# Kernel optimization log

Hardware: AMD Instinct MI355X
Metric: run time of the kernel (lower is better)

Reference implementation:

```python
import jax, jax.numpy as jnp
import numpy as np

SHAPES = ((28, 28, 28), (14, 14, 14), (7, 7, 7))  # (D,H,W) per level, hardcoded by offset_normalizer
M, L, P = 6, 3, 4  # n_heads, n_levels, n_points


def grid_sample_3d(vol, grid):
    """Trilinear grid sample, zeros padding, align_corners=False.
    vol: (B, C, D, H, W); grid: (B, Q, 3) with xyz in [-1,1] (x->W, y->H, z->D).
    Returns (B, C, Q)."""
    B, C, D, H, W = vol.shape
    x = ((grid[..., 0] + 1.0) * W - 1.0) * 0.5
    y = ((grid[..., 1] + 1.0) * H - 1.0) * 0.5
    z = ((grid[..., 2] + 1.0) * D - 1.0) * 0.5
    x0f = jnp.floor(x); y0f = jnp.floor(y); z0f = jnp.floor(z)
    fx = x - x0f; fy = y - y0f; fz = z - z0f
    x0 = x0f.astype(jnp.int32); y0 = y0f.astype(jnp.int32); z0 = z0f.astype(jnp.int32)
    flat = vol.reshape(B, C, D * H * W)
    out = jnp.zeros((B, C, grid.shape[1]), vol.dtype)
    for dz, wz in ((0, 1.0 - fz), (1, fz)):
        for dy, wy in ((0, 1.0 - fy), (1, fy)):
            for dx, wx in ((0, 1.0 - fx), (1, fx)):
                zi = z0 + dz; yi = y0 + dy; xi = x0 + dx
                valid = (zi >= 0) & (zi < D) & (yi >= 0) & (yi < H) & (xi >= 0) & (xi < W)
                idx = (jnp.clip(zi, 0, D - 1) * H + jnp.clip(yi, 0, H - 1)) * W + jnp.clip(xi, 0, W - 1)
                g = jnp.take_along_axis(flat, idx[:, None, :], axis=2)  # (B,C,Q)
                w = (wz * wy * wx) * valid.astype(vol.dtype)
                out = out + g * w[:, None, :]
    return out


def setup_inputs() -> dict:
    key = jax.random.key(0)
    ks = jax.random.split(key, 8)
    bs, Lq, d_model, image_dim, T = 1, 4096, 768, 1408, 2
    S = sum(d * h * w for d, h, w in SHAPES)  # 25039
    return {
        "query": jax.random.normal(ks[0], (bs, Lq, d_model), jnp.float32),
        "reference_points": jax.random.uniform(ks[1], (bs, Lq, 3), jnp.float32),
        "value": jax.random.normal(ks[2], (bs, T, S, image_dim), jnp.float32),
        "Wv": jax.random.normal(ks[3], (image_dim, d_model), jnp.float32) * 0.02,
        "bv": jnp.zeros((d_model,), jnp.float32),
        "Woff": jax.random.normal(ks[4], (d_model, M * T * L * P * 3), jnp.float32) * 0.02,
        "boff": jax.random.normal(ks[5], (M * T * L * P * 3,), jnp.float32) * 0.5,
        "Wa": jax.random.normal(ks[6], (d_model, M * T * L * P), jnp.float32) * 0.02,
        "ba": jnp.zeros((M * T * L * P,), jnp.float32),
        "Wo": jax.random.normal(ks[7], (d_model, d_model), jnp.float32) * 0.02,
        "bo": jnp.zeros((d_model,), jnp.float32),
    }


def reference(query, reference_points, value, Wv, bv, Woff, boff, Wa, ba, Wo, bo):
    N, Lq, d_model = query.shape
    T = value.shape[1]
    Dh = d_model // M
    # value projection + head split: (N,T,S,M,Dh)
    v = (value @ Wv + bv).reshape(N, T, -1, M, Dh)
    # sampling offsets and attention weights from query
    off = (query @ Woff + boff).reshape(N, Lq, M, T, L, P, 3)
    aw = jax.nn.softmax((query @ Wa + ba).reshape(N, Lq, M, T * L * P), axis=-1)
    aw = aw.reshape(N, Lq, M, T, L, P)
    normalizer = jnp.asarray([[28., 28., 28.], [14., 14., 14.], [7., 7., 7.]], query.dtype)
    loc = reference_points[:, :, None, None, None, None, :] + off / normalizer[None, None, None, None, :, None, :]
    grids = 2.0 * loc - 1.0  # (N,Lq,M,T,L,P,3)
    starts = [0]
    for (d, h, w) in SHAPES:
        starts.append(starts[-1] + d * h * w)
    sampled = []
    for l, (Dl, Hl, Wl) in enumerate(SHAPES):
        vl = v[:, :, starts[l]:starts[l + 1]]                       # (N,T,Sl,M,Dh)
        vl = vl.transpose(0, 1, 3, 4, 2).reshape(N * T * M, Dh, Dl, Hl, Wl)
        gl = grids[:, :, :, :, l].transpose(0, 3, 2, 1, 4, 5).reshape(N * T * M, Lq * P, 3)
        sampled.append(grid_sample_3d(vl, gl).reshape(N, T, M, Dh, Lq, P))
    s = jnp.stack(sampled, axis=5)                                  # (N,T,M,Dh,Lq,L,P)
    out = jnp.einsum('ntmdqlp,nqmtlp->nqmd', s, aw).reshape(N, Lq, M * Dh)
    return out @ Wo + bo
```

## Files before the change

kernel.cpp:

```cpp
#include <hip/hip_runtime.h>
#include <hip/hip_bf16.h>
#include <stdint.h>

#define LQ    4096
#define DMOD  768
#define IMGD  1408
#define TT    2
#define MM    6
#define LL    3
#define PP    4
#define DH    128
#define STOT  25039
#define OFFC  432
#define AWC   144
#define PROJC 576
#define NSAMP 24
#define NCORN 192

typedef __attribute__((ext_vector_type(8))) __bf16 bf16x8;
typedef __attribute__((ext_vector_type(4))) float  f32x4;

__device__ __forceinline__ void gl_lds16(const void* g, void* l) {
    __builtin_amdgcn_global_load_lds(
        (const __attribute__((address_space(1))) void*)g,
        (__attribute__((address_space(3))) void*)l, 16, 0, 0);
}

__global__ __launch_bounds__(256) void cvt_transpose(
    const float* __restrict__ W, __bf16* __restrict__ WT, int K, int N)
{
    __shared__ float tile[32][33];
    const int k0 = blockIdx.x * 32, n0 = blockIdx.y * 32;
    const int c = threadIdx.x & 31, r8 = threadIdx.x >> 5;
    #pragma unroll
    for (int i = 0; i < 4; ++i) {
        int r = r8 + i * 8;
        int k = k0 + r, n = n0 + c;
        tile[r][c] = (k < K && n < N) ? W[(size_t)k * N + n] : 0.f;
    }
    __syncthreads();
    #pragma unroll
    for (int i = 0; i < 4; ++i) {
        int r = r8 + i * 8;
        int n = n0 + r, k = k0 + c;
        if (n < N && k < K) WT[(size_t)n * K + k] = (__bf16)tile[c][r];
    }
}

__global__ void concat_bias(const float* __restrict__ boff,
                            const float* __restrict__ ba,
                            float* __restrict__ bcat)
{
    int i = blockIdx.x * blockDim.x + threadIdx.x;
    if (i < PROJC) bcat[i] = (i < OFFC) ? boff[i] : ba[i - OFFC];
}

__global__ __launch_bounds__(256) void cvt_bf16_kernel(
    const float* __restrict__ in, __bf16* __restrict__ out, int n8)
{
    const int stride = gridDim.x * blockDim.x;
    for (int i = blockIdx.x * blockDim.x + threadIdx.x; i < n8; i += stride) {
        const float4* p = (const float4*)(in + (size_t)i * 8);
        float4 v0 = p[0], v1 = p[1];
        bf16x8 o;
        o[0] = (__bf16)v0.x; o[1] = (__bf16)v0.y;
        o[2] = (__bf16)v0.z; o[3] = (__bf16)v0.w;
        o[4] = (__bf16)v1.x; o[5] = (__bf16)v1.y;
        o[6] = (__bf16)v1.z; o[7] = (__bf16)v1.w;
        *(bf16x8*)(out + (size_t)i * 8) = o;
    }
}

template<int AF32, int OUT_BF16, int SWZ>
__global__ __launch_bounds__(256, 3) void gemm_mfma(
    const void* __restrict__ Ap, const __bf16* __restrict__ BT,
    const float* __restrict__ bias, void* __restrict__ Cp,
    int M, int N, int K)
{
    __shared__ __bf16 As[2][128][32];
    __shared__ __bf16 Bs[2][128][32];

    const int tid  = threadIdx.x;
    const int lane = tid & 63;
    const int wave = tid >> 6;
    const int wm = (wave & 1) * 64;
    const int wn = (wave >> 1) * 64;

    int bx, by;
    if constexpr (SWZ > 0) {
        const int bid = blockIdx.x;
        const int xcd = bid & 7;
        const int slot = bid >> 3;
        const int ppx = (gridDim.x >> 3) / SWZ;
        const int pix = slot / SWZ;
        bx = slot - pix * SWZ;
        by = xcd * ppx + pix;
    } else {
        bx = blockIdx.x; by = blockIdx.y;
    }
    const int row0 = by * 128;
    const int col0 = bx * 128;

    const int fr = lane & 15;
    const int kq = lane >> 4;

    const int sr  = tid >> 1;
    const int kk0 = (tid & 1) * 16;

    float f[16];

    auto stageB = [&](int ki, int buf) {
        #pragma unroll
        for (int j = 0; j < 2; ++j) {
            const int g   = wave * 128 + j * 64 + lane;
            const int row = g >> 2, cir = g & 3;
            const __bf16* src = BT + (size_t)(col0 + row) * K + ki * 32 + cir * 8;
            gl_lds16(src, (char*)&Bs[buf][0][0] + (size_t)(wave * 128 + j * 64) * 16);
        }
    };
    auto stageA_lds = [&](int ki, int buf) {
        const __bf16* A = (const __bf16*)Ap;
        #pragma unroll
        for (int j = 0; j < 2; ++j) {
            const int g   = wave * 128 + j * 64 + lane;
            const int row = g >> 2, cir = g & 3;
            const __bf16* src = A + (size_t)(row0 + row) * K + ki * 32 + cir * 8;
            gl_lds16(src, (char*)&As[buf][0][0] + (size_t)(wave * 128 + j * 64) * 16);
        }
    };
    auto loadA_f32 = [&](int ki) {
        const float* A = (const float*)Ap;
        const int gm = row0 + sr;
        if (gm < M) {
            const float4* ap = (const float4*)(A + (size_t)gm * K + ki * 32 + kk0);
            #pragma unroll
            for (int i = 0; i < 4; ++i) {
                float4 v = ap[i];
                f[i*4+0] = v.x; f[i*4+1] = v.y; f[i*4+2] = v.z; f[i*4+3] = v.w;
            }
        } else {
            #pragma unroll
            for (int i = 0; i < 16; ++i) f[i] = 0.f;
        }
    };
    auto writeA = [&](int buf) {
        bf16x8 v0, v1;
        #pragma unroll
        for (int i = 0; i < 8; ++i) { v0[i] = (__bf16)f[i]; v1[i] = (__bf16)f[i+8]; }
        *(bf16x8*)&As[buf][sr][kk0]     = v0;
        *(bf16x8*)&As[buf][sr][kk0 + 8] = v1;
    };

    f32x4 acc[4][4] = {};
    const int nk = K >> 5;

    stageB(0, 0);
    if constexpr (AF32) { loadA_f32(0); writeA(0); }
    else                { stageA_lds(0, 0); }

    for (int i = 0; i < nk; ++i) {
        __syncthreads();
        const int cur = i & 1, nxt = cur ^ 1;
        const bool more = (i + 1) < nk;

        if (more) {
            stageB(i + 1, nxt);
            if constexpr (AF32) loadA_f32(i + 1);
            else                stageA_lds(i + 1, nxt);
        }

        bf16x8 a[4], b[4];
        #pragma unroll
        for (int mt = 0; mt < 4; ++mt) a[mt] = *(const bf16x8*)&As[cur][wm + mt*16 + fr][kq * 8];
        #pragma unroll
        for (int nt = 0; nt < 4; ++nt) b[nt] = *(const bf16x8*)&Bs[cur][wn + nt*16 + fr][kq * 8];
        #pragma unroll
        for (int mt = 0; mt < 4; ++mt)
            #pragma unroll
            for (int nt = 0; nt < 4; ++nt)
                acc[mt][nt] = __builtin_amdgcn_mfma_f32_16x16x32_bf16(
                    a[mt], b[nt], acc[mt][nt], 0, 0, 0);

        if constexpr (AF32) { if (more) writeA(nxt); }
    }

    const int col = lane & 15;
    const int rq  = (lane >> 4) * 4;
    #pragma unroll
    for (int mt = 0; mt < 4; ++mt) {
        #pragma unroll
        for (int r = 0; r < 4; ++r) {
            const int gm = row0 + wm + mt*16 + rq + r;
            if (gm >= M) continue;
            #pragma unroll
            for (int nt = 0; nt < 4; ++nt) {
                const int gn = col0 + wn + nt*16 + col;
                if (gn < N) {
                    float v = acc[mt][nt][r] + bias[gn];
                    if constexpr (OUT_BF16)
                        ((__bf16*)Cp)[(size_t)gm * N + gn] = (__bf16)v;
                    else
                        ((float*)Cp)[(size_t)gm * N + gn] = v;
                }
            }
        }
    }
}

__global__ __launch_bounds__(256) void sample_kernel(
    const float* __restrict__ refp,
    const float* __restrict__ proj,
    const __bf16* __restrict__ vbuf,
    __bf16* __restrict__ attn)
{
    const int wave = threadIdx.x >> 6;
    const int lane = threadIdx.x & 63;
    const int q = blockIdx.x * 4 + wave;
    const int m = blockIdx.y;

    __shared__ float    s_aw[4][NSAMP];
    __shared__ float    s_w[4][NCORN];
    __shared__ uint32_t s_o[4][NCORN];

    if (lane < NSAMP)
        s_aw[wave][lane] = proj[(size_t)q * PROJC + OFFC + m * NSAMP + lane];
    __syncthreads();

    if (lane < NSAMP) {
        float mx = -1e30f;
        #pragma unroll
        for (int i = 0; i < NSAMP; ++i) mx = fmaxf(mx, s_aw[wave][i]);
        float sum = 0.f;
        #pragma unroll
        for (int i = 0; i < NSAMP; ++i) sum += __expf(s_aw[wave][i] - mx);
        const float aww = __expf(s_aw[wave][lane] - mx) / sum;

        const int t = lane / 12;
        const int r = lane - t * 12;
        const int l = r >> 2;
        const int   Dl    = (l == 0) ? 28 : (l == 1) ? 14 : 7;
        const int   start = (l == 0) ? 0  : (l == 1) ? 21952 : 24696;
        const float fD    = (float)Dl;
        const int   base  = t * STOT + start;

        const float* op = proj + (size_t)q * PROJC + m * 72 + lane * 3;
        const float rx = refp[q*3+0], ry = refp[q*3+1], rz = refp[q*3+2];
        float x = rx * fD + op[0] - 0.5f;
        float y = ry * fD + op[1] - 0.5f;
        float z = rz * fD + op[2] - 0.5f;
        float xf = floorf(x), yf = floorf(y), zf = floorf(z);
        float fx = x - xf, fy = y - yf, fz = z - zf;
        int x0 = (int)xf, y0 = (int)yf, z0 = (int)zf;
        float wx[2] = {1.f - fx, fx}, wy[2] = {1.f - fy, fy}, wz[2] = {1.f - fz, fz};
        #pragma unroll
        for (int cc = 0; cc < 8; ++cc) {
            int dx = cc & 1, dy = (cc >> 1) & 1, dz = cc >> 2;
            int xi = x0 + dx, yi = y0 + dy, zi = z0 + dz;
            bool ok = (xi >= 0) & (xi < Dl) & (yi >= 0) & (yi < Dl) &
                      (zi >= 0) & (zi < Dl);
            float    w   = ok ? aww * wx[dx] * wy[dy] * wz[dz] : 0.f;
            uint32_t off = ok ? (uint32_t)(base + (zi * Dl + yi) * Dl + xi) * (768u * 2u) : 0u;
            s_w[wave][lane * 8 + cc] = w;
            s_o[wave][lane * 8 + cc] = off;
        }
    }
    __syncthreads();

    const int h = lane >> 5;
    const int c = lane & 31;
    const char* vb = (const char*)vbuf + ((size_t)m * 128 + c * 4) * 2;
    float a0 = 0.f, a1 = 0.f, a2 = 0.f, a3 = 0.f;
    #pragma unroll 4
    for (int i = 0; i < NCORN / 2; ++i) {
        const float    w   = s_w[wave][2 * i + h];
        const uint32_t off = s_o[wave][2 * i + h];
        const uint2 u = *(const uint2*)(vb + off);
        a0 += w * __uint_as_float(u.x << 16);
        a1 += w * __uint_as_float(u.x & 0xffff0000u);
        a2 += w * __uint_as_float(u.y << 16);
        a3 += w * __uint_as_float(u.y & 0xffff0000u);
    }
    a0 += __shfl_xor(a0, 32);
    a1 += __shfl_xor(a1, 32);
    a2 += __shfl_xor(a2, 32);
    a3 += __shfl_xor(a3, 32);

    if (h == 0) {
        union { __bf16 hh[4]; uint2 u; } pk;
        pk.hh[0] = (__bf16)a0; pk.hh[1] = (__bf16)a1;
        pk.hh[2] = (__bf16)a2; pk.hh[3] = (__bf16)a3;
        *(uint2*)((char*)attn + ((size_t)q * DMOD + m * 128 + c * 4) * 2) = pk.u;
    }
}

extern "C" void kernel_launch(void* const* d_in, const int* in_sizes, int n_in,
                              void* d_out, int out_size, void* d_ws, size_t ws_size,
                              hipStream_t stream) {
    const float* query = (const float*)d_in[0];
    const float* refp  = (const float*)d_in[1];
    const float* value = (const float*)d_in[2];
    const float* Wv    = (const float*)d_in[3];
    const float* bv    = (const float*)d_in[4];
    const float* Woff  = (const float*)d_in[5];
    const float* boff  = (const float*)d_in[6];
    const float* Wa    = (const float*)d_in[7];
    const float* ba    = (const float*)d_in[8];
    const float* Wo    = (const float*)d_in[9];
    const float* bo    = (const float*)d_in[10];
    float* out = (float*)d_out;

    const int    Mv      = TT * STOT;
    const size_t SZ_ABF  = (size_t)Mv * IMGD * 2;
    const size_t SZ_VBUF = (size_t)TT * STOT * DMOD * 2;
    const size_t SZ_PROJ = (size_t)LQ * PROJC * 4;
    const size_t SZ_ATTN = (size_t)LQ * DMOD * 2;
    const size_t SZ_WVT  = (size_t)IMGD * DMOD * 2;
    const size_t SZ_WCAT = (size_t)PROJC * DMOD * 2;
    const size_t SZ_WOT  = (size_t)DMOD * DMOD * 2;
    const size_t SZ_BCAT = (size_t)PROJC * 4;

    const size_t need_cvt = SZ_ABF + SZ_VBUF + SZ_PROJ + SZ_ATTN +
                            SZ_WVT + SZ_WCAT + SZ_WOT + SZ_BCAT;
    const bool use_cvtA = (ws_size >= need_cvt);

    char* p = (char*)d_ws;
    __bf16* abf = nullptr;
    if (use_cvtA) { abf = (__bf16*)p; p += SZ_ABF; }
    __bf16* vbuf  = (__bf16*)p; p += SZ_VBUF;
    float*  proj  = (float*)p;  p += SZ_PROJ;
    __bf16* attn  = (__bf16*)p; p += SZ_ATTN;
    __bf16* wvt   = (__bf16*)p; p += SZ_WVT;
    __bf16* wcatT = (__bf16*)p; p += SZ_WCAT;
    __bf16* woT   = (__bf16*)p; p += SZ_WOT;
    float*  bcat  = (float*)p;

    cvt_transpose<<<dim3((IMGD+31)/32, (DMOD+31)/32), 256, 0, stream>>>(Wv, wvt, IMGD, DMOD);
    cvt_transpose<<<dim3((DMOD+31)/32, (OFFC+31)/32), 256, 0, stream>>>(Woff, wcatT, DMOD, OFFC);
    cvt_transpose<<<dim3((DMOD+31)/32, (AWC +31)/32), 256, 0, stream>>>(Wa, wcatT + (size_t)OFFC * DMOD, DMOD, AWC);
    cvt_transpose<<<dim3((DMOD+31)/32, (DMOD+31)/32), 256, 0, stream>>>(Wo, woT, DMOD, DMOD);
    concat_bias<<<dim3(3), 256, 0, stream>>>(boff, ba, bcat);

    if (use_cvtA) {
        const int n8 = (int)(((size_t)Mv * IMGD) / 8);
        cvt_bf16_kernel<<<dim3(2048), 256, 0, stream>>>(value, abf, n8);
        gemm_mfma<0, 1, 6><<<dim3(2352), 256, 0, stream>>>(
            abf, wvt, bv, vbuf, Mv, DMOD, IMGD);
    } else {
        gemm_mfma<1, 1, 6><<<dim3(2352), 256, 0, stream>>>(
            value, wvt, bv, vbuf, Mv, DMOD, IMGD);
    }

    gemm_mfma<1, 0, 0><<<dim3((PROJC + 127) / 128, LQ / 128), 256, 0, stream>>>(
        query, wcatT, bcat, proj, LQ, PROJC, DMOD);

    sample_kernel<<<dim3(LQ / 4, MM), 256, 0, stream>>>(refp, proj, vbuf, attn);

    gemm_mfma<0, 0, 0><<<dim3(DMOD / 128, LQ / 128), 256, 0, stream>>>(
        attn, woT, bo, out, LQ, DMOD, DMOD);
}
```

Before: 739.6 us.

## Add 256x128 triple-buffered MFMA GEMM for value projection

Replaces the value-projection GEMM (bf16 A path) with a new kernel. It uses 512 threads, 256x128 output tiles, a K-step of 64, three LDS stages filled by direct global-to-LDS loads, XOR-swizzled LDS reads, the 16x16x32 bf16 MFMA and an XCD-aware block remap. The larger tiles raise data reuse per block and the deeper pipeline overlaps loads with MFMA work. In exchange, LDS use grows to about 144KB per block, which limits occupancy. The epilogue stores bf16 one element at a time and skips rows beyond M, since M is not a multiple of 256.

```diff
diff --git a/kernel.cpp b/kernel.cpp
--- a/kernel.cpp
+++ b/kernel.cpp
@@ -68,6 +68,118 @@
         o[4] = (__bf16)v1.x; o[5] = (__bf16)v1.y;
         o[6] = (__bf16)v1.z; o[7] = (__bf16)v1.w;
         *(bf16x8*)(out + (size_t)i * 8) = o;
+    }
+}
+
+#define G1_SPX 147
+
+__global__ __launch_bounds__(512, 2) void gemm_g1(
+    const __bf16* __restrict__ A, const __bf16* __restrict__ BT,
+    const float* __restrict__ bias, __bf16* __restrict__ C,
+    int M, int N, int K)
+{
+    __shared__ __bf16 As3[3][256][64];
+    __shared__ __bf16 Bs3[3][128][64];
+
+    const int tid  = threadIdx.x;
+    const int lane = tid & 63;
+    const int w    = tid >> 6;
+    const int wr   = w >> 1;
+    const int wc   = w & 1;
+
+    const int logical = (blockIdx.x & 7) * G1_SPX + (blockIdx.x >> 3);
+    const int panel = logical / 6;
+    const int colb  = logical - panel * 6;
+    const int row0  = panel * 256;
+    const int col0  = colb * 128;
+
+    const int fr = lane & 15;
+    const int kq = lane >> 4;
+
+    const int lr = lane >> 3;
+    const int qs = (lane & 7) ^ lr;
+
+    const __bf16* aSrc = A  + (size_t)(row0 + w * 32 + lr) * K + qs * 8;
+    const __bf16* bSrc = BT + (size_t)(col0 + w * 16 + lr) * K + qs * 8;
+
+    auto stage = [&](int kt, int r) {
+        const __bf16* as = aSrc + (size_t)kt * 64;
+        #pragma unroll
+        for (int j = 0; j < 4; ++j)
+            gl_lds16(as + (size_t)j * 8 * K,
+                     (char*)&As3[r][0][0] + (size_t)(w * 4 + j) * 1024);
+        const __bf16* bs = bSrc + (size_t)kt * 64;
+        #pragma unroll
+        for (int j = 0; j < 2; ++j)
+            gl_lds16(bs + (size_t)j * 8 * K,
+                     (char*)&Bs3[r][0][0] + (size_t)(w * 2 + j) * 1024);
+    };
+
+    f32x4 acc[4][4] = {};
+    const int nk = K >> 6;
+
+    stage(0, 0);
+    stage(1, 1);
+
+    const int sxa = (fr & 7) << 3;
+
+    int cur = 0;
+    for (int t = 0; t < nk; ++t) {
+        if (t + 1 < nk) asm volatile("s_waitcnt vmcnt(6) lgkmcnt(0)" ::: "memory");
+        else            asm volatile("s_waitcnt vmcnt(0) lgkmcnt(0)" ::: "memory");
+        __builtin_amdgcn_sched_barrier(0);
+        __builtin_amdgcn_s_barrier();
+        __builtin_amdgcn_sched_barrier(0);
+
+        if (t + 2 < nk) {
+            int stg = cur + 2; if (stg >= 3) stg -= 3;
+            stage(t + 2, stg);
+        }
+
+        bf16x8 a[4][2], b[4][2];
+        #pragma unroll
+        for (int mt = 0; mt < 4; ++mt) {
+            const int row = wr * 64 + mt * 16 + fr;
+            #pragma unroll
+            for (int h = 0; h < 2; ++h)
+                a[mt][h] = *(const bf16x8*)(&As3[cur][row][(h * 32 + kq * 8) ^ sxa]);
+        }
+        #pragma unroll
+        for (int nt = 0; nt < 4; ++nt) {
+            const int rowb = wc * 64 + nt * 16 + fr;
+            #pragma unroll
+            for (int h = 0; h < 2; ++h)
+                b[nt][h] = *(const bf16x8*)(&Bs3[cur][rowb][(h * 32 + kq * 8) ^ sxa]);
+        }
+
+        __builtin_amdgcn_s_setprio(1);
+        #pragma unroll
+        for (int mt = 0; mt < 4; ++mt)
+            #pragma unroll
+            for (int nt = 0; nt < 4; ++nt)
+                #pragma unroll
+                for (int h = 0; h < 2; ++h)
+                    acc[mt][nt] = __builtin_amdgcn_mfma_f32_16x16x32_bf16(
+                        a[mt][h], b[nt][h], acc[mt][nt], 0, 0, 0);
+        __builtin_amdgcn_s_setprio(0);
+
+        cur = (cur == 2) ? 0 : cur + 1;
+    }
+
+    const int col = lane & 15;
+    const int rq  = (lane >> 4) * 4;
+    #pragma unroll
+    for (int mt = 0; mt < 4; ++mt) {
+        #pragma unroll
+        for (int rr = 0; rr < 4; ++rr) {
+            const int gm = row0 + wr * 64 + mt * 16 + rq + rr;
+            if (gm >= M) continue;
+            #pragma unroll
+            for (int nt = 0; nt < 4; ++nt) {
+                const int gn = col0 + wc * 64 + nt * 16 + col;
+                C[(size_t)gm * N + gn] = (__bf16)(acc[mt][nt][rr] + bias[gn]);
+            }
+        }
     }
 }
 
@@ -343,7 +455,7 @@
     if (use_cvtA) {
         const int n8 = (int)(((size_t)Mv * IMGD) / 8);
         cvt_bf16_kernel<<<dim3(2048), 256, 0, stream>>>(value, abf, n8);
-        gemm_mfma<0, 1, 6><<<dim3(2352), 256, 0, stream>>>(
+        gemm_g1<<<dim3(1176), 512, 0, stream>>>(
             abf, wvt, bv, vbuf, Mv, DMOD, IMGD);
     } else {
         gemm_mfma<1, 1, 6><<<dim3(2352), 256, 0, stream>>>(
```

New measurement: 772.3 us. 1.04x slower.
